# Kernel tuning notes

Measured on AMD Instinct MI355X. Metric: run time of the kernel, lower is better.

The kernel has to match this reference:

```python
import jax, jax.numpy as jnp
import numpy as np

WINDOW = 50


def setup_inputs() -> dict:
    key = jax.random.key(0)
    ks = jax.random.split(key, 7)
    B, N = 32, 32768
    hidden = 32
    x = jax.random.normal(ks[0], (B, N), dtype=jnp.float32)
    # torch Linear weights stored as [in, out] (already transposed)
    w1 = jax.random.normal(ks[1], (4, 2 * hidden), dtype=jnp.float32) * (1.0 / np.sqrt(4))
    b1 = jnp.zeros((2 * hidden,), dtype=jnp.float32)
    w2 = jax.random.normal(ks[2], (2 * hidden, hidden), dtype=jnp.float32) * (1.0 / np.sqrt(2 * hidden))
    b2 = jnp.zeros((hidden,), dtype=jnp.float32)
    w3 = jax.random.normal(ks[3], (hidden, 2), dtype=jnp.float32) * (1.0 / np.sqrt(hidden))
    b3 = jnp.zeros((2,), dtype=jnp.float32)
    return {"x": x, "w1": w1, "b1": b1, "w2": w2, "b2": b2, "w3": w3, "b3": b3}


def reference(x, w1, b1, w2, b2, w3, b3):
    W = WINDOW
    B, N = x.shape
    M = N - W + 1
    # windows: [B, M, W] via gather (same layout as torch.unfold)
    idx = jnp.arange(M)[:, None] + jnp.arange(W)[None, :]  # [M, W]
    windows = x[:, idx]  # [B, M, W]
    mean = windows.mean(axis=-1, keepdims=True)
    centered = windows - mean
    # torch .std() is unbiased (ddof=1)
    var = (centered ** 2).sum(axis=-1, keepdims=True) / (W - 1)
    std = jnp.sqrt(var) + 1e-6
    skew = (centered ** 3).mean(axis=-1, keepdims=True) / std ** 3
    kurt = (centered ** 4).mean(axis=-1, keepdims=True) / std ** 4
    stats = jnp.concatenate([mean, std, skew, kurt], axis=-1)  # [B, M, 4]
    h = jax.nn.relu(stats @ w1 + b1)
    h = jax.nn.relu(h @ w2 + b2)
    params = h @ w3 + b3  # [B, M, 2]
    gamma = params[:, :, 0:1]
    beta = params[:, :, 1:2]
    normalized = centered / std
    reprojected = normalized * gamma + beta  # [B, M, W]
    return reprojected[:, :, W // 2]  # [B, M]
```

## Files before the change

### kernel.cpp

```cpp
#include <hip/hip_runtime.h>
#include <hip/hip_bf16.h>
#include <math.h>

#define WINDOW 50

typedef __attribute__((ext_vector_type(8))) short short8;
typedef __attribute__((ext_vector_type(4))) float f32x4;
typedef unsigned int uint;

union U8 { uint4 u; short8 s; };
union UF4 { uint4 u; f32x4 f; };
__device__ inline short8 as_s8(uint4 u) { U8 t; t.u = u; return t.s; }
__device__ inline f32x4  as_f4(uint4 u) { UF4 t; t.u = u; return t.f; }

__device__ inline uint pk2(float a, float b) {
    uint r;
    asm("v_cvt_pk_bf16_f32 %0, %1, %2" : "=v"(r) : "v"(a), "v"(b));
    return r;
}
__device__ inline float lo_f32(uint u) { return __uint_as_float(u << 16); }
__device__ inline float hi_f32(uint u) { return __uint_as_float(u & 0xffff0000u); }

#define LDS_FENCE() do { asm volatile("s_waitcnt lgkmcnt(0)" ::: "memory"); \
                         __builtin_amdgcn_sched_barrier(0); } while (0)

__global__ __launch_bounds__(64) void nsg_prep(
    const float* __restrict__ w1, const float* __restrict__ b1,
    const float* __restrict__ w2, const float* __restrict__ b2,
    const float* __restrict__ w3, uint4* __restrict__ ws)
{
    const int wl  = threadIdx.x;
    const int l15 = wl & 15;
    const int g   = wl >> 4;

    #pragma unroll
    for (int nt = 0; nt < 4; ++nt) {
        int n = nt * 16 + l15;
        float a = w1[n], b = w1[64 + n], c = w1[128 + n], d = w1[192 + n];
        uint hab = pk2(a, b), hcd = pk2(c, d);
        uint lab = pk2(a - lo_f32(hab), b - hi_f32(hab));
        uint lcd = pk2(c - lo_f32(hcd), d - hi_f32(hcd));
        float bb = b1[n];
        uint bh  = pk2(bb, 0.0f);
        uint bpk = pk2(bb, bb - lo_f32(bh));
        uint4 u;
        u.x = (g == 0) ? hab : (g == 1) ? lab : (g == 2) ? bpk : 0u;
        u.y = (g == 0) ? hcd : (g == 1) ? lcd : 0u;
        u.z = (g == 0) ? hab : (g == 1) ? lab : 0u;
        u.w = (g == 0) ? hcd : (g == 1) ? lcd : 0u;
        ws[nt * 64 + wl] = u;
    }
    #pragma unroll
    for (int nt = 0; nt < 4; ++nt) {
        #pragma unroll
        for (int mt = 0; mt < 2; ++mt) {
            int c = mt * 16 + l15;
            uint w[4];
            #pragma unroll
            for (int j = 0; j < 4; ++j) {
                float a = w2[(nt * 16 + g * 4 + j) * 32 + c];
                uint t = pk2(a, 0.0f);
                w[j] = pk2(a, a - lo_f32(t));
            }
            ws[(4 + nt * 2 + mt) * 64 + wl] = make_uint4(w[0], w[1], w[2], w[3]);
        }
    }
    #pragma unroll
    for (int mt = 0; mt < 2; ++mt)
        ws[(12 + mt) * 64 + wl] = *(const uint4*)(b2 + 16 * mt + 4 * g);
    #pragma unroll
    for (int mt = 0; mt < 2; ++mt)
        #pragma unroll
        for (int jj = 0; jj < 2; ++jj)
            ws[(14 + mt * 2 + jj) * 64 + wl] =
                *(const uint4*)(w3 + (16 * mt + 4 * g + 2 * jj) * 2);
}

__global__ __launch_bounds__(256, 2) void nsg_kernel(
    const float* __restrict__ x, const uint4* __restrict__ ws,
    const float* __restrict__ b3,
    float* __restrict__ out, int N, int M, int tiles)
{
    __shared__ float s_xw[4][128];
    __shared__ f32x4 s_ck[4][104];
    __shared__ uint4 s_stat[4][64];

    const int tid = threadIdx.x;
    const int wv  = tid >> 6;
    const int wl  = tid & 63;
    const int l15 = wl & 15;
    const int g   = wl >> 4;
    const int tile = blockIdx.x % tiles;
    const int row  = blockIdx.x / tiles;
    const int m0   = tile * 256 + wv * 64;

    const float* xr = x + (size_t)row * N;
    {
        int g0 = m0 + wl, g1 = m0 + 64 + wl;
        s_xw[wv][wl]      = (g0 < N) ? xr[g0] : 0.0f;
        s_xw[wv][64 + wl] = (g1 < N) ? xr[g1] : 0.0f;
    }

    short8 A1[4];
    uint4  A2[4][2];
    #pragma unroll
    for (int nt = 0; nt < 4; ++nt) A1[nt] = as_s8(ws[nt * 64 + wl]);
    #pragma unroll
    for (int nt = 0; nt < 4; ++nt)
        #pragma unroll
        for (int mt = 0; mt < 2; ++mt)
            A2[nt][mt] = ws[(4 + nt * 2 + mt) * 64 + wl];
    f32x4 b2r[2];
    #pragma unroll
    for (int mt = 0; mt < 2; ++mt) b2r[mt] = as_f4(ws[(12 + mt) * 64 + wl]);
    f32x4 w3q[4];
    #pragma unroll
    for (int p = 0; p < 4; ++p) w3q[p] = as_f4(ws[(14 + p) * 64 + wl]);
    const float b3g = b3[0], b3b = b3[1];
    const uint  K2  = (g == 2) ? 0x3F803F80u : 0u;
    const bool  gHi = (g >= 2);

    LDS_FENCE();

    f32x4 myC;
    {
        float S1 = 0.f, S2 = 0.f, S3 = 0.f, S4 = 0.f;
        #pragma unroll
        for (int i = 0; i < 10; ++i) {
            float v = s_xw[wv][wl + i], v2 = v * v;
            S1 += v; S2 += v2; S3 = fmaf(v2, v, S3); S4 = fmaf(v2, v2, S4);
        }
        myC = f32x4{S1, S2, S3, S4};
        s_ck[wv][wl] = myC;
    }
    if (wl < 40) {
        float S1 = 0.f, S2 = 0.f, S3 = 0.f, S4 = 0.f;
        #pragma unroll
        for (int i = 0; i < 10; ++i) {
            float v = s_xw[wv][64 + wl + i], v2 = v * v;
            S1 += v; S2 += v2; S3 = fmaf(v2, v, S3); S4 = fmaf(v2, v2, S4);
        }
        s_ck[wv][64 + wl] = f32x4{S1, S2, S3, S4};
    }
    LDS_FENCE();

    float nrm;
    {
        f32x4 ca = s_ck[wv][wl + 10], cb = s_ck[wv][wl + 20];
        f32x4 cc = s_ck[wv][wl + 30], cd = s_ck[wv][wl + 40];
        float S1 = myC[0] + ca[0] + cb[0] + cc[0] + cd[0];
        float S2 = myC[1] + ca[1] + cb[1] + cc[1] + cd[1];
        float S3 = myC[2] + ca[2] + cb[2] + cc[2] + cd[2];
        float S4 = myC[3] + ca[3] + cb[3] + cc[3] + cd[3];
        const float invW = 1.0f / (float)WINDOW;
        float mean = S1 * invW;
        float mu2  = mean * mean;
        float c2m = S2 - (float)WINDOW * mu2;
        float c3m = S3 - 3.0f * mean * S2 + 2.0f * (float)WINDOW * mu2 * mean;
        float c4m = S4 - 4.0f * mean * S3 + 6.0f * mu2 * S2
                      - 3.0f * (float)WINDOW * mu2 * mu2;
        float var    = c2m * (1.0f / (float)(WINDOW - 1));
        float sd     = sqrtf(var) + 1e-6f;
        float inv_sd = 1.0f / sd;
        float inv_sd2 = inv_sd * inv_sd;
        float skew = c3m * invW * inv_sd2 * inv_sd;
        float kurt = c4m * invW * inv_sd2 * inv_sd2;
        nrm = (s_xw[wv][wl + 25] - mean) * inv_sd;

        uint4 stp;
        uint h01 = pk2(mean, sd), h23 = pk2(skew, kurt);
        stp.x = h01;
        stp.y = h23;
        stp.z = pk2(mean - lo_f32(h01), sd - hi_f32(h01));
        stp.w = pk2(skew - lo_f32(h23), kurt - hi_f32(h23));
        s_stat[wv][wl] = stp;
    }
    LDS_FENCE();

    float ga = 0.f, be = 0.f;
    #pragma unroll
    for (int q = 0; q < 4; ++q) {
        uint4 st = s_stat[wv][q * 16 + l15];
        uint4 bq;
        bq.x = gHi ? K2 : st.x;
        bq.y = gHi ? 0u : st.y;
        bq.z = gHi ? 0u : st.z;
        bq.w = gHi ? 0u : st.w;
        short8 B1 = as_s8(bq);

        f32x4 c1[4];
        #pragma unroll
        for (int nt = 0; nt < 4; ++nt) {
            c1[nt] = f32x4{0.f, 0.f, 0.f, 0.f};
            c1[nt] = __builtin_amdgcn_mfma_f32_16x16x32_bf16(A1[nt], B1, c1[nt], 0, 0, 0);
        }

        f32x4 c2a[2] = { b2r[0], b2r[1] };
        f32x4 c2b[2] = { f32x4{0.f, 0.f, 0.f, 0.f}, f32x4{0.f, 0.f, 0.f, 0.f} };
        #pragma unroll
        for (int nt = 0; nt < 4; ++nt) {
            float r0 = fmaxf(c1[nt][0], 0.f), r1 = fmaxf(c1[nt][1], 0.f);
            float r2 = fmaxf(c1[nt][2], 0.f), r3 = fmaxf(c1[nt][3], 0.f);
            uint t01 = pk2(r0, r1), t23 = pk2(r2, r3);
            float h0 = lo_f32(t01), h1v = hi_f32(t01);
            float h2v = lo_f32(t23), h3v = hi_f32(t23);
            float l0 = r0 - h0, l1 = r1 - h1v, l2 = r2 - h2v, l3 = r3 - h3v;
            uint4 bb, bs;
            bb.x = pk2(h0, l0);  bb.y = pk2(h1v, l1);
            bb.z = pk2(h2v, l2); bb.w = pk2(h3v, l3);
            bs.x = pk2(l0, h0);  bs.y = pk2(l1, h1v);
            bs.z = pk2(l2, h2v); bs.w = pk2(l3, h3v);
            short8 B2 = as_s8(bb), B2s = as_s8(bs);
            #pragma unroll
            for (int mt = 0; mt < 2; ++mt) {
                c2a[mt] = __builtin_amdgcn_mfma_f32_16x16x32_bf16(as_s8(A2[nt][mt]), B2,  c2a[mt], 0, 0, 0);
                c2b[mt] = __builtin_amdgcn_mfma_f32_16x16x32_bf16(as_s8(A2[nt][mt]), B2s, c2b[mt], 0, 0, 0);
            }
        }

        float pg = 0.f, pb = 0.f;
        #pragma unroll
        for (int mt = 0; mt < 2; ++mt) {
            #pragma unroll
            for (int j = 0; j < 4; ++j) {
                float P = fmaxf(c2a[mt][j] + c2b[mt][j], 0.f);
                float wx = w3q[mt * 2 + (j >> 1)][(j & 1) * 2 + 0];
                float wy = w3q[mt * 2 + (j >> 1)][(j & 1) * 2 + 1];
                pg = fmaf(P, wx, pg);
                pb = fmaf(P, wy, pb);
            }
        }
        pg += __shfl_xor(pg, 16);
        pb += __shfl_xor(pb, 16);
        pg += __shfl_xor(pg, 32);
        pb += __shfl_xor(pb, 32);
        if (g == q) { ga = pg; be = pb; }
    }

    int m = m0 + wl;
    if (m < M)
        out[(size_t)row * M + m] = fmaf(nrm, ga + b3g, be + b3b);
}

extern "C" void kernel_launch(void* const* d_in, const int* in_sizes, int n_in,
                              void* d_out, int out_size, void* d_ws, size_t ws_size,
                              hipStream_t stream) {
    const float* x  = (const float*)d_in[0];
    const float* w1 = (const float*)d_in[1];
    const float* b1 = (const float*)d_in[2];
    const float* w2 = (const float*)d_in[3];
    const float* b2 = (const float*)d_in[4];
    const float* w3 = (const float*)d_in[5];
    const float* b3 = (const float*)d_in[6];
    float* out = (float*)d_out;
    uint4* ws = (uint4*)d_ws;

    const int N = 32768;
    const int B = in_sizes[0] / N;
    const int M = N - WINDOW + 1;
    const int tiles = (M + 255) / 256;

    nsg_prep<<<dim3(1), dim3(64), 0, stream>>>(w1, b1, w2, b2, w3, ws);
    nsg_kernel<<<dim3(B * tiles), dim3(256), 0, stream>>>(x, ws, b3, out, N, M, tiles);
}
```

Baseline: 39.46 us.

## Split fused kernel into separate stats and MLP kernels via global scratch

After: 51.25 us. +29.9%, slower.

```diff
diff --git a/kernel.cpp b/kernel.cpp
--- a/kernel.cpp
+++ b/kernel.cpp
@@ -76,30 +76,98 @@
                 *(const uint4*)(w3 + (16 * mt + 4 * g + 2 * jj) * 2);
 }
 
-__global__ __launch_bounds__(256, 2) void nsg_kernel(
-    const float* __restrict__ x, const uint4* __restrict__ ws,
-    const float* __restrict__ b3,
-    float* __restrict__ out, int N, int M, int tiles)
+__global__ __launch_bounds__(256) void nsg_stats(
+    const float* __restrict__ x, uint4* __restrict__ stp_o,
+    float* __restrict__ nrm_o, int N, int M)
 {
     __shared__ float s_xw[4][128];
     __shared__ f32x4 s_ck[4][104];
-    __shared__ uint4 s_stat[4][64];
+
+    const int tid = threadIdx.x;
+    const int wv  = tid >> 6;
+    const int wl  = tid & 63;
+    const int u   = blockIdx.x;
+    const int row = u >> 7;
+    const int m0  = (u & 127) * 256 + wv * 64;
+
+    const float* xr = x + (size_t)row * N;
+    {
+        int g0 = m0 + wl, g1 = m0 + 64 + wl;
+        s_xw[wv][wl]      = (g0 < N) ? xr[g0] : 0.0f;
+        s_xw[wv][64 + wl] = (g1 < N) ? xr[g1] : 0.0f;
+    }
+    LDS_FENCE();
+
+    f32x4 myC;
+    {
+        float S1 = 0.f, S2 = 0.f, S3 = 0.f, S4 = 0.f;
+        #pragma unroll
+        for (int i = 0; i < 10; ++i) {
+            float v = s_xw[wv][wl + i], v2 = v * v;
+            S1 += v; S2 += v2; S3 = fmaf(v2, v, S3); S4 = fmaf(v2, v2, S4);
+        }
+        myC = f32x4{S1, S2, S3, S4};
+        s_ck[wv][wl] = myC;
+    }
+    if (wl < 40) {
+        float S1 = 0.f, S2 = 0.f, S3 = 0.f, S4 = 0.f;
+        #pragma unroll
+        for (int i = 0; i < 10; ++i) {
+            float v = s_xw[wv][64 + wl + i], v2 = v * v;
+            S1 += v; S2 += v2; S3 = fmaf(v2, v, S3); S4 = fmaf(v2, v2, S4);
+        }
+        s_ck[wv][64 + wl] = f32x4{S1, S2, S3, S4};
+    }
+    LDS_FENCE();
+
+    f32x4 ca = s_ck[wv][wl + 10], cb = s_ck[wv][wl + 20];
+    f32x4 cc = s_ck[wv][wl + 30], cd = s_ck[wv][wl + 40];
+    float S1 = myC[0] + ca[0] + cb[0] + cc[0] + cd[0];
+    float S2 = myC[1] + ca[1] + cb[1] + cc[1] + cd[1];
+    float S3 = myC[2] + ca[2] + cb[2] + cc[2] + cd[2];
+    float S4 = myC[3] + ca[3] + cb[3] + cc[3] + cd[3];
+    const float invW = 1.0f / (float)WINDOW;
+    float mean = S1 * invW;
+    float mu2  = mean * mean;
+    float c2m = S2 - (float)WINDOW * mu2;
+    float c3m = S3 - 3.0f * mean * S2 + 2.0f * (float)WINDOW * mu2 * mean;
+    float c4m = S4 - 4.0f * mean * S3 + 6.0f * mu2 * S2
+                  - 3.0f * (float)WINDOW * mu2 * mu2;
+    float var    = c2m * (1.0f / (float)(WINDOW - 1));
+    float sd     = sqrtf(var) + 1e-6f;
+    float inv_sd = 1.0f / sd;
+    float inv_sd2 = inv_sd * inv_sd;
+    float skew = c3m * invW * inv_sd2 * inv_sd;
+    float kurt = c4m * invW * inv_sd2 * inv_sd2;
+    float nrm  = (s_xw[wv][wl + 25] - mean) * inv_sd;
+
+    uint4 stp;
+    uint h01 = pk2(mean, sd), h23 = pk2(skew, kurt);
+    stp.x = h01;
+    stp.y = h23;
+    stp.z = pk2(mean - lo_f32(h01), sd - hi_f32(h01));
+    stp.w = pk2(skew - lo_f32(h23), kurt - hi_f32(h23));
+
+    int m = m0 + wl;
+    if (m < M) {
+        int w = (row << 15) + m;
+        stp_o[w] = stp;
+        nrm_o[w] = nrm;
+    }
+}
+
+__global__ __launch_bounds__(256, 2) void nsg_mlp(
+    const uint4* __restrict__ ws, const uint4* __restrict__ stp_i,
+    const float* __restrict__ nrm_i, const float* __restrict__ b3,
+    float* __restrict__ out, int M)
+{
+    __shared__ uint4 s_w3[4][64];
 
     const int tid = threadIdx.x;
     const int wv  = tid >> 6;
     const int wl  = tid & 63;
     const int l15 = wl & 15;
     const int g   = wl >> 4;
-    const int tile = blockIdx.x % tiles;
-    const int row  = blockIdx.x / tiles;
-    const int m0   = tile * 256 + wv * 64;
-
-    const float* xr = x + (size_t)row * N;
-    {
-        int g0 = m0 + wl, g1 = m0 + 64 + wl;
-        s_xw[wv][wl]      = (g0 < N) ? xr[g0] : 0.0f;
-        s_xw[wv][64 + wl] = (g1 < N) ? xr[g1] : 0.0f;
-    }
 
     short8 A1[4];
     uint4  A2[4][2];
@@ -113,133 +181,82 @@
     f32x4 b2r[2];
     #pragma unroll
     for (int mt = 0; mt < 2; ++mt) b2r[mt] = as_f4(ws[(12 + mt) * 64 + wl]);
-    f32x4 w3q[4];
-    #pragma unroll
-    for (int p = 0; p < 4; ++p) w3q[p] = as_f4(ws[(14 + p) * 64 + wl]);
+
+    if (wv == 0) {
+        #pragma unroll
+        for (int p = 0; p < 4; ++p) s_w3[p][wl] = ws[(14 + p) * 64 + wl];
+    }
     const float b3g = b3[0], b3b = b3[1];
     const uint  K2  = (g == 2) ? 0x3F803F80u : 0u;
     const bool  gHi = (g >= 2);
-
-    LDS_FENCE();
-
-    f32x4 myC;
-    {
-        float S1 = 0.f, S2 = 0.f, S3 = 0.f, S4 = 0.f;
-        #pragma unroll
-        for (int i = 0; i < 10; ++i) {
-            float v = s_xw[wv][wl + i], v2 = v * v;
-            S1 += v; S2 += v2; S3 = fmaf(v2, v, S3); S4 = fmaf(v2, v2, S4);
-        }
-        myC = f32x4{S1, S2, S3, S4};
-        s_ck[wv][wl] = myC;
-    }
-    if (wl < 40) {
-        float S1 = 0.f, S2 = 0.f, S3 = 0.f, S4 = 0.f;
-        #pragma unroll
-        for (int i = 0; i < 10; ++i) {
-            float v = s_xw[wv][64 + wl + i], v2 = v * v;
-            S1 += v; S2 += v2; S3 = fmaf(v2, v, S3); S4 = fmaf(v2, v2, S4);
-        }
-        s_ck[wv][64 + wl] = f32x4{S1, S2, S3, S4};
-    }
-    LDS_FENCE();
-
-    float nrm;
-    {
-        f32x4 ca = s_ck[wv][wl + 10], cb = s_ck[wv][wl + 20];
-        f32x4 cc = s_ck[wv][wl + 30], cd = s_ck[wv][wl + 40];
-        float S1 = myC[0] + ca[0] + cb[0] + cc[0] + cd[0];
-        float S2 = myC[1] + ca[1] + cb[1] + cc[1] + cd[1];
-        float S3 = myC[2] + ca[2] + cb[2] + cc[2] + cd[2];
-        float S4 = myC[3] + ca[3] + cb[3] + cc[3] + cd[3];
-        const float invW = 1.0f / (float)WINDOW;
-        float mean = S1 * invW;
-        float mu2  = mean * mean;
-        float c2m = S2 - (float)WINDOW * mu2;
-        float c3m = S3 - 3.0f * mean * S2 + 2.0f * (float)WINDOW * mu2 * mean;
-        float c4m = S4 - 4.0f * mean * S3 + 6.0f * mu2 * S2
-                      - 3.0f * (float)WINDOW * mu2 * mu2;
-        float var    = c2m * (1.0f / (float)(WINDOW - 1));
-        float sd     = sqrtf(var) + 1e-6f;
-        float inv_sd = 1.0f / sd;
-        float inv_sd2 = inv_sd * inv_sd;
-        float skew = c3m * invW * inv_sd2 * inv_sd;
-        float kurt = c4m * invW * inv_sd2 * inv_sd2;
-        nrm = (s_xw[wv][wl + 25] - mean) * inv_sd;
-
-        uint4 stp;
-        uint h01 = pk2(mean, sd), h23 = pk2(skew, kurt);
-        stp.x = h01;
-        stp.y = h23;
-        stp.z = pk2(mean - lo_f32(h01), sd - hi_f32(h01));
-        stp.w = pk2(skew - lo_f32(h23), kurt - hi_f32(h23));
-        s_stat[wv][wl] = stp;
-    }
-    LDS_FENCE();
-
-    float ga = 0.f, be = 0.f;
-    #pragma unroll
-    for (int q = 0; q < 4; ++q) {
-        uint4 st = s_stat[wv][q * 16 + l15];
-        uint4 bq;
-        bq.x = gHi ? K2 : st.x;
-        bq.y = gHi ? 0u : st.y;
-        bq.z = gHi ? 0u : st.z;
-        bq.w = gHi ? 0u : st.w;
-        short8 B1 = as_s8(bq);
-
-        f32x4 c1[4];
-        #pragma unroll
-        for (int nt = 0; nt < 4; ++nt) {
-            c1[nt] = f32x4{0.f, 0.f, 0.f, 0.f};
-            c1[nt] = __builtin_amdgcn_mfma_f32_16x16x32_bf16(A1[nt], B1, c1[nt], 0, 0, 0);
-        }
-
-        f32x4 c2a[2] = { b2r[0], b2r[1] };
-        f32x4 c2b[2] = { f32x4{0.f, 0.f, 0.f, 0.f}, f32x4{0.f, 0.f, 0.f, 0.f} };
-        #pragma unroll
-        for (int nt = 0; nt < 4; ++nt) {
-            float r0 = fmaxf(c1[nt][0], 0.f), r1 = fmaxf(c1[nt][1], 0.f);
-            float r2 = fmaxf(c1[nt][2], 0.f), r3 = fmaxf(c1[nt][3], 0.f);
-            uint t01 = pk2(r0, r1), t23 = pk2(r2, r3);
-            float h0 = lo_f32(t01), h1v = hi_f32(t01);
-            float h2v = lo_f32(t23), h3v = hi_f32(t23);
-            float l0 = r0 - h0, l1 = r1 - h1v, l2 = r2 - h2v, l3 = r3 - h3v;
-            uint4 bb, bs;
-            bb.x = pk2(h0, l0);  bb.y = pk2(h1v, l1);
-            bb.z = pk2(h2v, l2); bb.w = pk2(h3v, l3);
-            bs.x = pk2(l0, h0);  bs.y = pk2(l1, h1v);
-            bs.z = pk2(l2, h2v); bs.w = pk2(l3, h3v);
-            short8 B2 = as_s8(bb), B2s = as_s8(bs);
+    __syncthreads();
+
+    const int wbase = (int)blockIdx.x * 1024 + wv * 256;
+    const int row   = wbase >> 15;
+    float* outr = out + (size_t)row * M;
+
+    #pragma unroll 1
+    for (int qq = 0; qq < 4; ++qq) {
+        float ga = 0.f, be = 0.f;
+        #pragma unroll
+        for (int sub = 0; sub < 4; ++sub) {
+            uint4 st = stp_i[wbase + qq * 64 + sub * 16 + l15];
+            uint4 bq;
+            bq.x = gHi ? K2 : st.x;
+            bq.y = gHi ? 0u : st.y;
+            bq.z = gHi ? 0u : st.z;
+            bq.w = gHi ? 0u : st.w;
+            short8 B1 = as_s8(bq);
+
+            f32x4 c2a[2] = { b2r[0], b2r[1] };
+            f32x4 c2b[2] = { f32x4{0.f, 0.f, 0.f, 0.f}, f32x4{0.f, 0.f, 0.f, 0.f} };
+            #pragma unroll
+            for (int nt = 0; nt < 4; ++nt) {
+                f32x4 c1 = f32x4{0.f, 0.f, 0.f, 0.f};
+                c1 = __builtin_amdgcn_mfma_f32_16x16x32_bf16(A1[nt], B1, c1, 0, 0, 0);
+                float r0 = fmaxf(c1[0], 0.f), r1 = fmaxf(c1[1], 0.f);
+                float r2 = fmaxf(c1[2], 0.f), r3 = fmaxf(c1[3], 0.f);
+                uint t01 = pk2(r0, r1), t23 = pk2(r2, r3);
+                float h0 = lo_f32(t01), h1v = hi_f32(t01);
+                float h2v = lo_f32(t23), h3v = hi_f32(t23);
+                float l0 = r0 - h0, l1 = r1 - h1v, l2 = r2 - h2v, l3 = r3 - h3v;
+                uint4 bb, bs;
+                bb.x = pk2(h0, l0);  bb.y = pk2(h1v, l1);
+                bb.z = pk2(h2v, l2); bb.w = pk2(h3v, l3);
+                bs.x = pk2(l0, h0);  bs.y = pk2(l1, h1v);
+                bs.z = pk2(l2, h2v); bs.w = pk2(l3, h3v);
+                short8 B2 = as_s8(bb), B2s = as_s8(bs);
+                #pragma unroll
+                for (int mt = 0; mt < 2; ++mt) {
+                    c2a[mt] = __builtin_amdgcn_mfma_f32_16x16x32_bf16(as_s8(A2[nt][mt]), B2,  c2a[mt], 0, 0, 0);
+                    c2b[mt] = __builtin_amdgcn_mfma_f32_16x16x32_bf16(as_s8(A2[nt][mt]), B2s, c2b[mt], 0, 0, 0);
+                }
+            }
+            float pg = 0.f, pb = 0.f;
             #pragma unroll
             for (int mt = 0; mt < 2; ++mt) {
-                c2a[mt] = __builtin_amdgcn_mfma_f32_16x16x32_bf16(as_s8(A2[nt][mt]), B2,  c2a[mt], 0, 0, 0);
-                c2b[mt] = __builtin_amdgcn_mfma_f32_16x16x32_bf16(as_s8(A2[nt][mt]), B2s, c2b[mt], 0, 0, 0);
+                #pragma unroll
+                for (int jj = 0; jj < 2; ++jj) {
+                    f32x4 wq = as_f4(s_w3[mt * 2 + jj][wl]);
+                    #pragma unroll
+                    for (int h = 0; h < 2; ++h) {
+                        float P = fmaxf(c2a[mt][jj * 2 + h] + c2b[mt][jj * 2 + h], 0.f);
+                        pg = fmaf(P, wq[h * 2 + 0], pg);
+                        pb = fmaf(P, wq[h * 2 + 1], pb);
+                    }
+                }
             }
-        }
-
-        float pg = 0.f, pb = 0.f;
-        #pragma unroll
-        for (int mt = 0; mt < 2; ++mt) {
-            #pragma unroll
-            for (int j = 0; j < 4; ++j) {
-                float P = fmaxf(c2a[mt][j] + c2b[mt][j], 0.f);
-                float wx = w3q[mt * 2 + (j >> 1)][(j & 1) * 2 + 0];
-                float wy = w3q[mt * 2 + (j >> 1)][(j & 1) * 2 + 1];
-                pg = fmaf(P, wx, pg);
-                pb = fmaf(P, wy, pb);
-            }
-        }
-        pg += __shfl_xor(pg, 16);
-        pb += __shfl_xor(pb, 16);
-        pg += __shfl_xor(pg, 32);
-        pb += __shfl_xor(pb, 32);
-        if (g == q) { ga = pg; be = pb; }
-    }
-
-    int m = m0 + wl;
-    if (m < M)
-        out[(size_t)row * M + m] = fmaf(nrm, ga + b3g, be + b3b);
+            pg += __shfl_xor(pg, 16);
+            pb += __shfl_xor(pb, 16);
+            pg += __shfl_xor(pg, 32);
+            pb += __shfl_xor(pb, 32);
+            if (g == sub) { ga = pg; be = pb; }
+        }
+        int w = wbase + qq * 64 + wl;
+        int m = w & 32767;
+        if (m < M)
+            outr[m] = fmaf(nrm_i[w], ga + b3g, be + b3b);
+    }
 }
 
 extern "C" void kernel_launch(void* const* d_in, const int* in_sizes, int n_in,
@@ -253,13 +270,15 @@
     const float* w3 = (const float*)d_in[5];
     const float* b3 = (const float*)d_in[6];
     float* out = (float*)d_out;
-    uint4* ws = (uint4*)d_ws;
 
     const int N = 32768;
-    const int B = in_sizes[0] / N;
     const int M = N - WINDOW + 1;
-    const int tiles = (M + 255) / 256;
+
+    uint4* ws    = (uint4*)d_ws;
+    uint4* stp   = (uint4*)((char*)d_ws + 64 * 1024);
+    float* nrm   = (float*)((char*)d_ws + 64 * 1024 + (size_t)16 * 1024 * 1024);
 
     nsg_prep<<<dim3(1), dim3(64), 0, stream>>>(w1, b1, w2, b2, w3, ws);
-    nsg_kernel<<<dim3(B * tiles), dim3(256), 0, stream>>>(x, ws, b3, out, N, M, tiles);
-}
+    nsg_stats<<<dim3(4096), dim3(256), 0, stream>>>(x, stp, nrm, N, M);
+    nsg_mlp<<<dim3(1024), dim3(256), 0, stream>>>(ws, stp, nrm, b3, out, M);
+}
```
